# Kernel tuning notes

Hardware: AMD Instinct MI355X
Metric: run time of the kernel (lower is better)

The kernel has to match this reference:

```python
import jax, jax.numpy as jnp
import numpy as np

B, S, C, HD = 2, 1024, 1024, 64
H = C // HD  # 16 heads
E = 4
EPS = 1e-5


def _ln(x, g, b):
    m = jnp.mean(x, axis=-1, keepdims=True)
    v = jnp.mean(jnp.square(x - m), axis=-1, keepdims=True)
    return (x - m) / jnp.sqrt(v + EPS) * g + b


def setup_inputs() -> dict:
    key = jax.random.key(0)
    ks = jax.random.split(key, 16)
    s = 0.02
    return {
        "fwd_x": jax.random.normal(ks[0], (B, S + 1, C), jnp.float32),
        "bwd_x": jax.random.normal(ks[1], (B, S + 1, C), jnp.float32),
        "pos_embed": jax.random.normal(ks[2], (S, HD), jnp.float32) * 0.01,
        "ln1_g": jnp.ones((C,), jnp.float32),
        "ln1_b": jnp.zeros((C,), jnp.float32),
        "Wq": jax.random.normal(ks[3], (C, C), jnp.float32) * s,
        "bq": jnp.zeros((C,), jnp.float32),
        "Wk": jax.random.normal(ks[4], (C, C), jnp.float32) * s,
        "bk": jnp.zeros((C,), jnp.float32),
        "Wv": jax.random.normal(ks[5], (C, C), jnp.float32) * s,
        "bv": jnp.zeros((C,), jnp.float32),
        "Wo": jax.random.normal(ks[6], (C, C), jnp.float32) * s,
        "bo": jnp.zeros((C,), jnp.float32),
        "ln2_g": jnp.ones((C,), jnp.float32),
        "ln2_b": jnp.zeros((C,), jnp.float32),
        "mlp_g": jnp.ones((C,), jnp.float32),
        "mlp_b": jnp.zeros((C,), jnp.float32),
        "W1": jax.random.normal(ks[7], (C, E * C), jnp.float32) * s,
        "b1": jnp.zeros((E * C,), jnp.float32),
        "W2": jax.random.normal(ks[8], (E * C, C), jnp.float32) * s,
        "b2": jnp.zeros((C,), jnp.float32),
    }


def reference(fwd_x, bwd_x, pos_embed, ln1_g, ln1_b, Wq, bq, Wk, bk, Wv, bv,
              Wo, bo, ln2_g, ln2_b, mlp_g, mlp_b, W1, b1, W2, b2):
    f = fwd_x[:, :-1, :]   # [B, S, C]
    r = bwd_x[:, 1:, :]    # [B, S, C]
    comb = (f + r) * np.float32(1.0 / np.sqrt(2.0))

    all_embed = jnp.concatenate([f, r], axis=1)       # [B, 2S, C]
    cx = _ln(comb, ln1_g, ln1_b)
    ae = _ln(all_embed, ln1_g, ln1_b)

    q = (cx @ Wq + bq).reshape(B, S, H, HD)
    k = (ae @ Wk + bk).reshape(B, 2 * S, H, HD)
    v = (ae @ Wv + bv).reshape(B, 2 * S, H, HD)

    pos2 = jnp.concatenate([pos_embed, pos_embed], axis=0)  # [2S, HD]
    k = k + pos2[None, :, None, :]
    q = (q + pos_embed[None, :, None, :]) * np.float32(1.0 / np.sqrt(HD))

    logits = jnp.einsum('bqhd,bkhd->bhqk', q, k)      # [B, H, S, 2S]

    qi = jnp.arange(S)[:, None]
    ki = jnp.arange(S)[None, :]
    l2r = ki <= qi   # causal (keys up to and incl. q) on first half
    r2l = ki >= qi   # anti-causal on second half
    mask = jnp.concatenate([l2r, r2l], axis=-1)        # [S, 2S]

    neg = jnp.finfo(logits.dtype).min
    attn = jax.nn.softmax(jnp.where(mask[None, None], logits, neg), axis=-1)

    o = jnp.einsum('bhqk,bkhd->bqhd', attn, v).reshape(B, S, C)
    o = o @ Wo + bo

    x = comb + o
    h = _ln(_ln(x, ln2_g, ln2_b), mlp_g, mlp_b)
    m = jax.nn.gelu(h @ W1 + b1, approximate=False) @ W2 + b2
    return x + m
```

## Files before the change

### kernel.cpp

```cpp
#include <hip/hip_runtime.h>
#include <hip/hip_bf16.h>
#include <cstdint>

#define DI __device__ __forceinline__

typedef unsigned short u16;
typedef __bf16 bf16x8 __attribute__((ext_vector_type(8)));
typedef float f32x4 __attribute__((ext_vector_type(4)));

constexpr int Bc  = 2;
constexpr int Sc  = 1024;
constexpr int Cc  = 1024;
constexpr int Hc  = 16;
constexpr int HDc = 64;
constexpr int S2c = 2048;
constexpr int ECc = 4096;
constexpr int BSc  = Bc * Sc;
constexpr int BS2c = Bc * S2c;

constexpr int EPI_KV = 0, EPI_Q = 1, EPI_O = 3, EPI_GELU = 4, EPI_FINAL = 5, EPI_PART = 6;

DI u16 f2b(float f) {
  __hip_bfloat16 h = __float2bfloat16(f);
  u16 u;
  __builtin_memcpy(&u, &h, 2);
  return u;
}

DI u16 f2b_fast(float f) {
  uint32_t u;
  __builtin_memcpy(&u, &f, 4);
  return (u16)((u + 0x8000u) >> 16);
}

DI void glds16(const void* g, void* l) {
  auto* lp = reinterpret_cast<__attribute__((address_space(3))) uint32_t*>(
      reinterpret_cast<uintptr_t>(l));
  __builtin_amdgcn_global_load_lds(
      reinterpret_cast<const __attribute__((address_space(1))) uint32_t*>(
          reinterpret_cast<uintptr_t>(g)),
      lp, 16, 0, 0);
}

DI f32x4 mfma16(bf16x8 a, bf16x8 b, f32x4 c) {
  return __builtin_amdgcn_mfma_f32_16x16x32_bf16(a, b, c, 0, 0, 0);
}

#define PIPE_WAIT(N)                                            \
  do {                                                          \
    asm volatile("s_waitcnt vmcnt(" #N ")" ::: "memory");       \
    __builtin_amdgcn_sched_barrier(0);                          \
  } while (0)
#define PIPE_BAR()                                              \
  do {                                                          \
    __builtin_amdgcn_s_barrier();                               \
    __builtin_amdgcn_sched_barrier(0);                          \
  } while (0)

__global__ __launch_bounds__(256) void transpose4_kernel(const float* __restrict__ Wq,
                                                         const float* __restrict__ Wk,
                                                         const float* __restrict__ Wv,
                                                         const float* __restrict__ Wo,
                                                         u16* __restrict__ WqT,
                                                         u16* __restrict__ WkvT,
                                                         u16* __restrict__ WoT) {
  __shared__ float tile[32][33];
  const int z = blockIdx.z;
  const float* W = (z == 0) ? Wq : (z == 1) ? Wk : (z == 2) ? Wv : Wo;
  u16* WT = (z == 0) ? WqT : (z == 1) ? WkvT : (z == 2) ? (WkvT + (size_t)Cc * Cc) : WoT;
  const int bx = blockIdx.x, by = blockIdx.y;
  const int tx = threadIdx.x, ty = threadIdx.y;
  const int c = bx * 32 + tx;
#pragma unroll
  for (int i = ty; i < 32; i += 8) tile[i][tx] = W[(size_t)(by * 32 + i) * Cc + c];
  __syncthreads();
#pragma unroll
  for (int i = ty; i < 32; i += 8)
    WT[(size_t)(bx * 32 + i) * Cc + by * 32 + tx] = f2b(tile[tx][i]);
}

__global__ __launch_bounds__(256) void transpose_kernel(const float* __restrict__ W,
                                                        u16* __restrict__ WT, int R, int Cn) {
  __shared__ float tile[32][33];
  const int bx = blockIdx.x, by = blockIdx.y;
  const int tx = threadIdx.x, ty = threadIdx.y;
  const int c = bx * 32 + tx;
#pragma unroll
  for (int i = ty; i < 32; i += 8) tile[i][tx] = W[(size_t)(by * 32 + i) * Cn + c];
  __syncthreads();
#pragma unroll
  for (int i = ty; i < 32; i += 8)
    WT[(size_t)(bx * 32 + i) * R + by * 32 + tx] = f2b(tile[tx][i]);
}

__global__ __launch_bounds__(256) void prep_ln_kernel(
    const float* __restrict__ fwd, const float* __restrict__ bwd, const float* __restrict__ g,
    const float* __restrict__ be, float* __restrict__ comb, u16* __restrict__ cx,
    u16* __restrict__ ae) {
  __shared__ float red[2][4];
  const int row = blockIdx.x, tid = threadIdx.x;
  const int c = tid * 4;
  float4 x;
  u16* dst;
  if (row < BSc) {
    const int b = row >> 10, s = row & (Sc - 1);
    const float4 f = *(const float4*)(fwd + ((size_t)(b * (Sc + 1) + s)) * Cc + c);
    const float4 r = *(const float4*)(bwd + ((size_t)(b * (Sc + 1) + s + 1)) * Cc + c);
    const float k = 0.70710678118654752f;
    x.x = (f.x + r.x) * k; x.y = (f.y + r.y) * k;
    x.z = (f.z + r.z) * k; x.w = (f.w + r.w) * k;
    *(float4*)(comb + (size_t)row * Cc + c) = x;
    dst = cx + (size_t)row * Cc;
  } else {
    const int idx = row - BSc;
    const int b = idx >> 11, t = idx & (S2c - 1);
    const float* src = (t < Sc) ? (fwd + ((size_t)(b * (Sc + 1) + t)) * Cc)
                                : (bwd + ((size_t)(b * (Sc + 1) + (t - Sc) + 1)) * Cc);
    x = *(const float4*)(src + c);
    dst = ae + (size_t)idx * Cc;
  }
  float s1 = x.x + x.y + x.z + x.w;
  float s2 = x.x * x.x + x.y * x.y + x.z * x.z + x.w * x.w;
  for (int off = 32; off; off >>= 1) { s1 += __shfl_down(s1, off); s2 += __shfl_down(s2, off); }
  if ((tid & 63) == 0) { red[0][tid >> 6] = s1; red[1][tid >> 6] = s2; }
  __syncthreads();
  s1 = red[0][0] + red[0][1] + red[0][2] + red[0][3];
  s2 = red[1][0] + red[1][1] + red[1][2] + red[1][3];
  const float mean = s1 * (1.0f / Cc);
  const float rstd = rsqrtf(s2 * (1.0f / Cc) - mean * mean + 1e-5f);
  const float4 gv = *(const float4*)(g + c);
  const float4 bv = *(const float4*)(be + c);
  ushort4 o;
  o.x = f2b((x.x - mean) * rstd * gv.x + bv.x);
  o.y = f2b((x.y - mean) * rstd * gv.y + bv.y);
  o.z = f2b((x.z - mean) * rstd * gv.z + bv.z);
  o.w = f2b((x.w - mean) * rstd * gv.w + bv.w);
  *(ushort4*)(dst + c) = o;
}

__global__ __launch_bounds__(256) void ln2_kernel(const float* __restrict__ x,
                                                  const float* __restrict__ g2,
                                                  const float* __restrict__ b2,
                                                  const float* __restrict__ gm,
                                                  const float* __restrict__ bm,
                                                  u16* __restrict__ h) {
  __shared__ float red[2][4];
  const int row = blockIdx.x, tid = threadIdx.x;
  const int c = tid * 4;
  const float4 v = *(const float4*)(x + (size_t)row * Cc + c);
  float s1 = v.x + v.y + v.z + v.w;
  float s2 = v.x * v.x + v.y * v.y + v.z * v.z + v.w * v.w;
  for (int off = 32; off; off >>= 1) { s1 += __shfl_down(s1, off); s2 += __shfl_down(s2, off); }
  if ((tid & 63) == 0) { red[0][tid >> 6] = s1; red[1][tid >> 6] = s2; }
  __syncthreads();
  s1 = red[0][0] + red[0][1] + red[0][2] + red[0][3];
  s2 = red[1][0] + red[1][1] + red[1][2] + red[1][3];
  float mean = s1 * (1.0f / Cc);
  float rstd = rsqrtf(s2 * (1.0f / Cc) - mean * mean + 1e-5f);
  const float4 ga = *(const float4*)(g2 + c);
  const float4 ba = *(const float4*)(b2 + c);
  const float t0 = (v.x - mean) * rstd * ga.x + ba.x;
  const float t1 = (v.y - mean) * rstd * ga.y + ba.y;
  const float t2 = (v.z - mean) * rstd * ga.z + ba.z;
  const float t3 = (v.w - mean) * rstd * ga.w + ba.w;
  s1 = t0 + t1 + t2 + t3;
  s2 = t0 * t0 + t1 * t1 + t2 * t2 + t3 * t3;
  for (int off = 32; off; off >>= 1) { s1 += __shfl_down(s1, off); s2 += __shfl_down(s2, off); }
  __syncthreads();
  if ((tid & 63) == 0) { red[0][tid >> 6] = s1; red[1][tid >> 6] = s2; }
  __syncthreads();
  s1 = red[0][0] + red[0][1] + red[0][2] + red[0][3];
  s2 = red[1][0] + red[1][1] + red[1][2] + red[1][3];
  mean = s1 * (1.0f / Cc);
  rstd = rsqrtf(s2 * (1.0f / Cc) - mean * mean + 1e-5f);
  const float4 gb = *(const float4*)(gm + c);
  const float4 bb = *(const float4*)(bm + c);
  ushort4 o;
  o.x = f2b((t0 - mean) * rstd * gb.x + bb.x);
  o.y = f2b((t1 - mean) * rstd * gb.y + bb.y);
  o.z = f2b((t2 - mean) * rstd * gb.z + bb.z);
  o.w = f2b((t3 - mean) * rstd * gb.w + bb.w);
  *(ushort4*)(h + (size_t)row * Cc + c) = o;
}

template <int EPI, int SK>
__global__ __launch_bounds__(512) void gemm_kernel(
    const u16* __restrict__ A, const u16* __restrict__ BT, const float* __restrict__ bias,
    const float* __restrict__ bias2, const float* __restrict__ pos,
    u16* __restrict__ outb, u16* __restrict__ out2, float* __restrict__ pbuf,
    int M, int N, int K) {
  __shared__ u16 A0s[128 * 32], A1s[128 * 32], A2s[128 * 32], A3s[128 * 32];
  __shared__ u16 B0s[128 * 32], B1s[128 * 32], B2s[128 * 32], B3s[128 * 32];
  const int tid = threadIdx.x;
  const int w = tid >> 6, lane = tid & 63, quad = lane >> 4, r16 = lane & 15;
  const int bm = blockIdx.y * 128, bn = blockIdx.x * 128;
  const int wm = (w >> 2) * 64, wn = (w & 3) * 32;
  const int Ks = K / SK, kb0 = blockIdx.z * Ks;

  const int srow = tid >> 2, scol = (tid & 3) * 8;
  const u16* aP = A + (size_t)(bm + srow) * K + kb0 + scol;
  const u16* bP = BT + (size_t)(bn + srow) * K + kb0 + scol;
  const int stg = (w * 16) * 32;

  f32x4 acc[4][2] = {};

  auto STAGE = [&](u16* Ad, u16* Bd, int t) {
    const int ko = t * 32;
    glds16(aP + ko, Ad + stg);
    glds16(bP + ko, Bd + stg);
  };
  auto COMPUTE = [&](const u16* As, const u16* Bs) {
    bf16x8 af[4], bfr[2];
#pragma unroll
    for (int i = 0; i < 4; i++)
      af[i] = *reinterpret_cast<const bf16x8*>(&As[(wm + i * 16 + r16) * 32 + quad * 8]);
#pragma unroll
    for (int i = 0; i < 2; i++)
      bfr[i] = *reinterpret_cast<const bf16x8*>(&Bs[(wn + i * 16 + r16) * 32 + quad * 8]);
#pragma unroll
    for (int mi = 0; mi < 4; mi++)
#pragma unroll
      for (int ni = 0; ni < 2; ni++) acc[mi][ni] = mfma16(af[mi], bfr[ni], acc[mi][ni]);
  };

  const int NT = Ks / 32;
  STAGE(A0s, B0s, 0);
  STAGE(A1s, B1s, 1);
  for (int t = 0; t < NT; t += 4) {
    if (t + 2 < NT) { STAGE(A2s, B2s, t + 2); PIPE_WAIT(4); }
    else if (t + 1 < NT) PIPE_WAIT(2);
    else PIPE_WAIT(0);
    PIPE_BAR();
    COMPUTE(A0s, B0s);
    if (t + 3 < NT) { STAGE(A3s, B3s, t + 3); PIPE_WAIT(4); }
    else if (t + 2 < NT) PIPE_WAIT(2);
    else PIPE_WAIT(0);
    PIPE_BAR();
    COMPUTE(A1s, B1s);
    if (t + 4 < NT) { STAGE(A0s, B0s, t + 4); PIPE_WAIT(4); }
    else if (t + 3 < NT) PIPE_WAIT(2);
    else PIPE_WAIT(0);
    PIPE_BAR();
    COMPUTE(A2s, B2s);
    if (t + 5 < NT) { STAGE(A1s, B1s, t + 5); PIPE_WAIT(4); }
    else if (t + 4 < NT) PIPE_WAIT(2);
    else PIPE_WAIT(0);
    PIPE_BAR();
    COMPUTE(A3s, B3s);
  }

#pragma unroll
  for (int mi = 0; mi < 4; mi++) {
#pragma unroll
    for (int ni = 0; ni < 2; ni++) {
      const int col = bn + wn + ni * 16 + r16;
      const int row0 = bm + wm + mi * 16 + quad * 4;
      if constexpr (EPI == EPI_PART) {
        float* pb = pbuf + (size_t)blockIdx.z * M * N;
#pragma unroll
        for (int r = 0; r < 4; r++) pb[(size_t)(row0 + r) * N + col] = acc[mi][ni][r];
      } else if constexpr (EPI == EPI_KV) {
        if (col < Cc) {
#pragma unroll
          for (int r = 0; r < 4; r++) {
            const int row = row0 + r;
            const int key = row & (S2c - 1);
            const float y =
                acc[mi][ni][r] + bias[col] + pos[(key & (Sc - 1)) * HDc + (col & 63)];
            outb[(size_t)row * Cc + col] = f2b(y);
          }
        } else {
          const int c2 = col - Cc;
          const int h = c2 >> 6, d = c2 & 63;
          const int b = row0 >> 11, key0 = row0 & (S2c - 1);
          const float bb = bias2[c2];
          ushort4 pk;
          pk.x = f2b(acc[mi][ni][0] + bb);
          pk.y = f2b(acc[mi][ni][1] + bb);
          pk.z = f2b(acc[mi][ni][2] + bb);
          pk.w = f2b(acc[mi][ni][3] + bb);
          *(ushort4*)&out2[(((size_t)(b * Hc + h) * HDc + d) << 11) + key0] = pk;
        }
      } else {
#pragma unroll
        for (int r = 0; r < 4; r++) {
          const float y = acc[mi][ni][r] + bias[col];
          outb[(size_t)(row0 + r) * N + col] =
              f2b(0.5f * y * (1.0f + erff(y * 0.70710678118654752f)));
        }
      }
    }
  }
}

template <int EPI, int SK>
__global__ __launch_bounds__(256) void reduce_kernel(const float* __restrict__ pbuf,
                                                     const float* __restrict__ bias,
                                                     const float* __restrict__ pos,
                                                     const float* __restrict__ addsrc,
                                                     u16* __restrict__ outb,
                                                     float* __restrict__ outf, int M, int N) {
  const size_t flat = ((size_t)blockIdx.x * 256 + threadIdx.x) * 4;
  const int row = (int)(flat / N), col = (int)(flat % N);
  const size_t MN = (size_t)M * N;
  float4 s = *(const float4*)(pbuf + flat);
#pragma unroll
  for (int z = 1; z < SK; z++) {
    const float4 v = *(const float4*)(pbuf + z * MN + flat);
    s.x += v.x; s.y += v.y; s.z += v.z; s.w += v.w;
  }
  const float4 bv = *(const float4*)(bias + col);
  s.x += bv.x; s.y += bv.y; s.z += bv.z; s.w += bv.w;
  if constexpr (EPI == EPI_Q) {
    const int sq = row & (Sc - 1), d = col & 63;
    const float4 pv = *(const float4*)(pos + sq * HDc + d);
    constexpr float sc = 0.180336880111120426f;
    ushort4 o;
    o.x = f2b((s.x + pv.x) * sc);
    o.y = f2b((s.y + pv.y) * sc);
    o.z = f2b((s.z + pv.z) * sc);
    o.w = f2b((s.w + pv.w) * sc);
    *(ushort4*)(outb + flat) = o;
  } else {
    const float4 av = *(const float4*)(addsrc + flat);
    float4 o;
    o.x = s.x + av.x; o.y = s.y + av.y; o.z = s.z + av.z; o.w = s.w + av.w;
    *(float4*)(outf + flat) = o;
  }
}

__global__ __launch_bounds__(256) void attn_kernel(const u16* __restrict__ qb,
                                                   const u16* __restrict__ kb,
                                                   const u16* __restrict__ vT,
                                                   u16* __restrict__ ob) {
  const int bh = blockIdx.x;
  const int qt = blockIdx.y;
  const int b = bh >> 4, head = bh & 15;
  const int tid = threadIdx.x;
  const int w = tid >> 6, lane = tid & 63, quad = lane >> 4, r16 = lane & 15;

  __shared__ u16 K0s[4096], K1s[4096], K2s[4096], K3s[4096];
  __shared__ u16 V0s[4096], V1s[4096], V2s[4096], V3s[4096];
  __shared__ u16 Ps[4][16 * 68];
  u16* ps = Ps[w];

  const int qw = qt * 64 + w * 16;

  bf16x8 aq[2];
  {
    const u16* qp = qb + ((size_t)((b * Sc + qw + r16) * Hc + head)) * HDc + quad * 8;
    aq[0] = *(const bf16x8*)qp;
    aq[1] = *(const bf16x8*)(qp + 32);
  }

  const size_t krow = (size_t)Hc * HDc;
  const u16* kbase = kb + ((size_t)b * S2c * Hc + head) * HDc;
  const u16* vbase = vT + ((size_t)(b * Hc + head)) * HDc * S2c;

  const int srow = w * 16 + (lane >> 2);
  const int scol = (lane & 3) * 8;
  const int stg = w * 16 * 32;
  const u16* kS = kbase + (size_t)srow * krow + scol;
  const u16* vS = vbase + (size_t)srow * S2c + scol;

  f32x4 o_acc[4] = {};
  float lsum[4] = {};

  auto K0OF = [&](int p) -> int { return (p <= qt) ? p * 64 : Sc + (p - 1) * 64; };

  auto STAGE = [&](u16* Kd, u16* Vd, int p) {
    const int k0 = K0OF(p);
    glds16(kS + (size_t)k0 * krow, Kd + stg);
    glds16(kS + (size_t)k0 * krow + 32, Kd + 2048 + stg);
    glds16(vS + k0, Vd + stg);
    glds16(vS + k0 + 32, Vd + 2048 + stg);
  };

  auto COMPUTE = [&](const u16* Kc, const u16* Vc, int p) {
    const int k0 = K0OF(p);
    f32x4 sacc[4] = {};
#pragma unroll
    for (int ks = 0; ks < 2; ks++)
#pragma unroll
      for (int ni = 0; ni < 4; ni++) {
        const bf16x8 bk = *(const bf16x8*)&Kc[ks * 2048 + (ni * 16 + r16) * 32 + quad * 8];
        sacc[ni] = mfma16(aq[ks], bk, sacc[ni]);
      }
    const int mode = (p == qt) ? 1 : ((p == qt + 1) ? 2 : 0);
#pragma unroll
    for (int r = 0; r < 4; r++) {
      const int qrow = qw + quad * 4 + r;
#pragma unroll
      for (int ni = 0; ni < 4; ni++) {
        float s = sacc[ni][r];
        if (mode == 1) { const int key = k0 + ni * 16 + r16; if (key > qrow) s = -128.0f; }
        else if (mode == 2) { const int key = k0 - Sc + ni * 16 + r16; if (key < qrow) s = -128.0f; }
        const float pe = __builtin_amdgcn_exp2f(s);
        lsum[r] += pe;
        ps[(quad * 4 + r) * 68 + ni * 16 + r16] = f2b_fast(pe);
      }
    }
#pragma unroll
    for (int ks = 0; ks < 2; ks++) {
      const bf16x8 ap = *(const bf16x8*)(&ps[r16 * 68 + ks * 32 + quad * 8]);
#pragma unroll
      for (int ni = 0; ni < 4; ni++) {
        const bf16x8 bv_ = *(const bf16x8*)&Vc[ks * 2048 + (ni * 16 + r16) * 32 + quad * 8];
        o_acc[ni] = mfma16(ap, bv_, o_acc[ni]);
      }
    }
  };

  constexpr int NU = 17;
  STAGE(K0s, V0s, 0);
  STAGE(K1s, V1s, 1);
  for (int t = 0; t < NU; t += 4) {
    {
      if (t + 2 < NU) { STAGE(K2s, V2s, t + 2); PIPE_WAIT(8); }
      else if (t + 1 < NU) PIPE_WAIT(4);
      else PIPE_WAIT(0);
      PIPE_BAR();
      COMPUTE(K0s, V0s, t);
    }
    if (t + 1 < NU) {
      if (t + 3 < NU) { STAGE(K3s, V3s, t + 3); PIPE_WAIT(8); }
      else if (t + 2 < NU) PIPE_WAIT(4);
      else PIPE_WAIT(0);
      PIPE_BAR();
      COMPUTE(K1s, V1s, t + 1);
    }
    if (t + 2 < NU) {
      if (t + 4 < NU) { STAGE(K0s, V0s, t + 4); PIPE_WAIT(8); }
      else if (t + 3 < NU) PIPE_WAIT(4);
      else PIPE_WAIT(0);
      PIPE_BAR();
      COMPUTE(K2s, V2s, t + 2);
    }
    if (t + 3 < NU) {
      if (t + 5 < NU) { STAGE(K1s, V1s, t + 5); PIPE_WAIT(8); }
      else if (t + 4 < NU) PIPE_WAIT(4);
      else PIPE_WAIT(0);
      PIPE_BAR();
      COMPUTE(K3s, V3s, t + 3);
    }
  }

#pragma unroll
  for (int r = 0; r < 4; r++) {
    float l = lsum[r];
    l += __shfl_xor(l, 1);
    l += __shfl_xor(l, 2);
    l += __shfl_xor(l, 4);
    l += __shfl_xor(l, 8);
    lsum[r] = 1.0f / l;
  }
#pragma unroll
  for (int r = 0; r < 4; r++) {
    u16* od = ob + ((size_t)((b * Sc + qw + quad * 4 + r) * Hc + head)) * HDc;
#pragma unroll
    for (int ni = 0; ni < 4; ni++) od[ni * 16 + r16] = f2b(o_acc[ni][r] * lsum[r]);
  }
}

extern "C" void kernel_launch(void* const* d_in, const int* in_sizes, int n_in, void* d_out,
                              int out_size, void* d_ws, size_t ws_size, hipStream_t stream) {
  const float* fwd = (const float*)d_in[0];
  const float* bwd = (const float*)d_in[1];
  const float* pos = (const float*)d_in[2];
  const float* ln1g = (const float*)d_in[3];
  const float* ln1b = (const float*)d_in[4];
  const float* Wq = (const float*)d_in[5];
  const float* bq = (const float*)d_in[6];
  const float* Wk = (const float*)d_in[7];
  const float* bk = (const float*)d_in[8];
  const float* Wv = (const float*)d_in[9];
  const float* bv = (const float*)d_in[10];
  const float* Wo = (const float*)d_in[11];
  const float* bo = (const float*)d_in[12];
  const float* ln2g = (const float*)d_in[13];
  const float* ln2b = (const float*)d_in[14];
  const float* mlpg = (const float*)d_in[15];
  const float* mlpb = (const float*)d_in[16];
  const float* W1 = (const float*)d_in[17];
  const float* b1 = (const float*)d_in[18];
  const float* W2 = (const float*)d_in[19];
  const float* b2 = (const float*)d_in[20];

  char* p = (char*)d_ws;
  auto alloc = [&](size_t bytes) -> char* {
    char* r = p;
    p += (bytes + 255) & ~(size_t)255;
    return r;
  };
  float* comb = (float*)alloc((size_t)BSc * Cc * 4);
  float* xbuf = (float*)alloc((size_t)BSc * Cc * 4);
  u16* cx = (u16*)alloc((size_t)BSc * Cc * 2);
  u16* ae = (u16*)alloc((size_t)BS2c * Cc * 2);
  u16* qbuf = (u16*)alloc((size_t)BSc * Cc * 2);
  u16* kbuf = (u16*)alloc((size_t)BS2c * Cc * 2);
  u16* vTb = (u16*)alloc((size_t)BS2c * Cc * 2);
  u16* obuf = (u16*)alloc((size_t)BSc * Cc * 2);
  u16* hb = (u16*)alloc((size_t)BSc * Cc * 2);
  u16* midb = (u16*)alloc((size_t)BSc * ECc * 2);
  float* pbuf = (float*)alloc((size_t)4 * BSc * Cc * 4);
  u16* WqT = (u16*)alloc((size_t)Cc * Cc * 2);
  u16* WkvT = (u16*)alloc((size_t)2 * Cc * Cc * 2);
  u16* WoT = (u16*)alloc((size_t)Cc * Cc * 2);
  u16* W1T = (u16*)alloc((size_t)ECc * Cc * 2);
  u16* W2T = (u16*)alloc((size_t)Cc * ECc * 2);

  const dim3 tb(32, 8);
  transpose4_kernel<<<dim3(32, 32, 4), tb, 0, stream>>>(Wq, Wk, Wv, Wo, WqT, WkvT, WoT);
  transpose_kernel<<<dim3(128, 32), tb, 0, stream>>>(W1, W1T, Cc, ECc);
  transpose_kernel<<<dim3(32, 128), tb, 0, stream>>>(W2, W2T, ECc, Cc);

  prep_ln_kernel<<<BSc + BS2c, 256, 0, stream>>>(fwd, bwd, ln1g, ln1b, comb, cx, ae);

  gemm_kernel<EPI_PART, 4><<<dim3(Cc / 128, BSc / 128, 4), 512, 0, stream>>>(
      cx, WqT, nullptr, nullptr, nullptr, nullptr, nullptr, pbuf, BSc, Cc, Cc);
  reduce_kernel<EPI_Q, 4><<<(BSc * Cc / 4) / 256, 256, 0, stream>>>(
      pbuf, bq, pos, nullptr, qbuf, nullptr, BSc, Cc);

  gemm_kernel<EPI_KV, 1><<<dim3(2 * Cc / 128, BS2c / 128, 1), 512, 0, stream>>>(
      ae, WkvT, bk, bv, pos, kbuf, vTb, nullptr, BS2c, 2 * Cc, Cc);

  attn_kernel<<<dim3(Bc * Hc, Sc / 64), 256, 0, stream>>>(qbuf, kbuf, vTb, obuf);

  gemm_kernel<EPI_PART, 4><<<dim3(Cc / 128, BSc / 128, 4), 512, 0, stream>>>(
      obuf, WoT, nullptr, nullptr, nullptr, nullptr, nullptr, pbuf, BSc, Cc, Cc);
  reduce_kernel<EPI_O, 4><<<(BSc * Cc / 4) / 256, 256, 0, stream>>>(
      pbuf, bo, nullptr, comb, nullptr, xbuf, BSc, Cc);

  ln2_kernel<<<BSc, 256, 0, stream>>>(xbuf, ln2g, ln2b, mlpg, mlpb, hb);

  gemm_kernel<EPI_GELU, 1><<<dim3(ECc / 128, BSc / 128, 1), 512, 0, stream>>>(
      hb, W1T, b1, nullptr, nullptr, midb, nullptr, nullptr, BSc, ECc, Cc);

  gemm_kernel<EPI_PART, 4><<<dim3(Cc / 128, BSc / 128, 4), 512, 0, stream>>>(
      midb, W2T, nullptr, nullptr, nullptr, nullptr, nullptr, pbuf, BSc, Cc, ECc);
  reduce_kernel<EPI_FINAL, 4><<<(BSc * Cc / 4) / 256, 256, 0, stream>>>(
      pbuf, b2, nullptr, xbuf, nullptr, (float*)d_out, BSc, Cc);
}
```

Measured before the change: 322.0 us.

## Fuse O-projection split-K reduce into LN2 and use 1024-thread GEMM blocks

Merges the split-K reduction of the output projection (with bias and residual add) into the double-LayerNorm kernel, dropping one launch and one full read of the residual buffer. Separately, the GEMM moves from 512 to 1024 threads per 128x128 tile. Each wave now computes a 32x32 sub-tile instead of 64x32, and the A and B staging loads are split between two thread halves, so the pipeline wait counts are halved. The larger blocks raise wave count per tile but halve per-wave MFMA work and may cost occupancy or register headroom.

```diff
diff --git a/kernel.cpp b/kernel.cpp
--- a/kernel.cpp
+++ b/kernel.cpp
@@ -18,7 +18,7 @@
 constexpr int BSc  = Bc * Sc;
 constexpr int BS2c = Bc * S2c;
 
-constexpr int EPI_KV = 0, EPI_Q = 1, EPI_O = 3, EPI_GELU = 4, EPI_FINAL = 5, EPI_PART = 6;
+constexpr int EPI_KV = 0, EPI_Q = 1, EPI_GELU = 4, EPI_FINAL = 5, EPI_PART = 6;
 
 DI u16 f2b(float f) {
   __hip_bfloat16 h = __float2bfloat16(f);
@@ -138,18 +138,28 @@
   *(ushort4*)(dst + c) = o;
 }
 
-__global__ __launch_bounds__(256) void ln2_kernel(const float* __restrict__ x,
-                                                  const float* __restrict__ g2,
-                                                  const float* __restrict__ b2,
-                                                  const float* __restrict__ gm,
-                                                  const float* __restrict__ bm,
-                                                  u16* __restrict__ h) {
+__global__ __launch_bounds__(256) void reduceO_ln2_kernel(
+    const float* __restrict__ pbuf, const float* __restrict__ bo,
+    const float* __restrict__ comb, const float* __restrict__ g2,
+    const float* __restrict__ b2, const float* __restrict__ gm,
+    const float* __restrict__ bm, float* __restrict__ xbuf, u16* __restrict__ hb) {
   __shared__ float red[2][4];
   const int row = blockIdx.x, tid = threadIdx.x;
   const int c = tid * 4;
-  const float4 v = *(const float4*)(x + (size_t)row * Cc + c);
-  float s1 = v.x + v.y + v.z + v.w;
-  float s2 = v.x * v.x + v.y * v.y + v.z * v.z + v.w * v.w;
+  constexpr size_t MN = (size_t)BSc * Cc;
+  const size_t flat = (size_t)row * Cc + c;
+  float4 s = *(const float4*)(pbuf + flat);
+#pragma unroll
+  for (int z = 1; z < 4; z++) {
+    const float4 v = *(const float4*)(pbuf + z * MN + flat);
+    s.x += v.x; s.y += v.y; s.z += v.z; s.w += v.w;
+  }
+  const float4 bv = *(const float4*)(bo + c);
+  const float4 cv = *(const float4*)(comb + flat);
+  s.x += bv.x + cv.x; s.y += bv.y + cv.y; s.z += bv.z + cv.z; s.w += bv.w + cv.w;
+  *(float4*)(xbuf + flat) = s;
+  float s1 = s.x + s.y + s.z + s.w;
+  float s2 = s.x * s.x + s.y * s.y + s.z * s.z + s.w * s.w;
   for (int off = 32; off; off >>= 1) { s1 += __shfl_down(s1, off); s2 += __shfl_down(s2, off); }
   if ((tid & 63) == 0) { red[0][tid >> 6] = s1; red[1][tid >> 6] = s2; }
   __syncthreads();
@@ -159,10 +169,10 @@
   float rstd = rsqrtf(s2 * (1.0f / Cc) - mean * mean + 1e-5f);
   const float4 ga = *(const float4*)(g2 + c);
   const float4 ba = *(const float4*)(b2 + c);
-  const float t0 = (v.x - mean) * rstd * ga.x + ba.x;
-  const float t1 = (v.y - mean) * rstd * ga.y + ba.y;
-  const float t2 = (v.z - mean) * rstd * ga.z + ba.z;
-  const float t3 = (v.w - mean) * rstd * ga.w + ba.w;
+  const float t0 = (s.x - mean) * rstd * ga.x + ba.x;
+  const float t1 = (s.y - mean) * rstd * ga.y + ba.y;
+  const float t2 = (s.z - mean) * rstd * ga.z + ba.z;
+  const float t3 = (s.w - mean) * rstd * ga.w + ba.w;
   s1 = t0 + t1 + t2 + t3;
   s2 = t0 * t0 + t1 * t1 + t2 * t2 + t3 * t3;
   for (int off = 32; off; off >>= 1) { s1 += __shfl_down(s1, off); s2 += __shfl_down(s2, off); }
@@ -180,11 +190,11 @@
   o.y = f2b((t1 - mean) * rstd * gb.y + bb.y);
   o.z = f2b((t2 - mean) * rstd * gb.z + bb.z);
   o.w = f2b((t3 - mean) * rstd * gb.w + bb.w);
-  *(ushort4*)(h + (size_t)row * Cc + c) = o;
+  *(ushort4*)(hb + flat) = o;
 }
 
 template <int EPI, int SK>
-__global__ __launch_bounds__(512) void gemm_kernel(
+__global__ __launch_bounds__(1024) void gemm_kernel(
     const u16* __restrict__ A, const u16* __restrict__ BT, const float* __restrict__ bias,
     const float* __restrict__ bias2, const float* __restrict__ pos,
     u16* __restrict__ outb, u16* __restrict__ out2, float* __restrict__ pbuf,
@@ -194,31 +204,30 @@
   const int tid = threadIdx.x;
   const int w = tid >> 6, lane = tid & 63, quad = lane >> 4, r16 = lane & 15;
   const int bm = blockIdx.y * 128, bn = blockIdx.x * 128;
-  const int wm = (w >> 2) * 64, wn = (w & 3) * 32;
+  const int wm = ((w >> 2) & 3) * 32, wn = (w & 3) * 32;
   const int Ks = K / SK, kb0 = blockIdx.z * Ks;
 
-  const int srow = tid >> 2, scol = (tid & 3) * 8;
-  const u16* aP = A + (size_t)(bm + srow) * K + kb0 + scol;
-  const u16* bP = BT + (size_t)(bn + srow) * K + kb0 + scol;
-  const int stg = (w * 16) * 32;
-
-  f32x4 acc[4][2] = {};
+  const bool isB = (tid >= 512);
+  const int t2 = tid & 511;
+  const int srow = t2 >> 2, scol = (t2 & 3) * 8;
+  const u16* gP =
+      (isB ? BT + (size_t)(bn + srow) * K : A + (size_t)(bm + srow) * K) + kb0 + scol;
+  const int stg = ((w & 7) * 16) * 32;
+
+  f32x4 acc[2][2] = {};
 
   auto STAGE = [&](u16* Ad, u16* Bd, int t) {
-    const int ko = t * 32;
-    glds16(aP + ko, Ad + stg);
-    glds16(bP + ko, Bd + stg);
+    glds16(gP + t * 32, (isB ? Bd : Ad) + stg);
   };
   auto COMPUTE = [&](const u16* As, const u16* Bs) {
-    bf16x8 af[4], bfr[2];
-#pragma unroll
-    for (int i = 0; i < 4; i++)
+    bf16x8 af[2], bfr[2];
+#pragma unroll
+    for (int i = 0; i < 2; i++) {
       af[i] = *reinterpret_cast<const bf16x8*>(&As[(wm + i * 16 + r16) * 32 + quad * 8]);
-#pragma unroll
-    for (int i = 0; i < 2; i++)
       bfr[i] = *reinterpret_cast<const bf16x8*>(&Bs[(wn + i * 16 + r16) * 32 + quad * 8]);
-#pragma unroll
-    for (int mi = 0; mi < 4; mi++)
+    }
+#pragma unroll
+    for (int mi = 0; mi < 2; mi++)
 #pragma unroll
       for (int ni = 0; ni < 2; ni++) acc[mi][ni] = mfma16(af[mi], bfr[ni], acc[mi][ni]);
   };
@@ -227,30 +236,30 @@
   STAGE(A0s, B0s, 0);
   STAGE(A1s, B1s, 1);
   for (int t = 0; t < NT; t += 4) {
-    if (t + 2 < NT) { STAGE(A2s, B2s, t + 2); PIPE_WAIT(4); }
-    else if (t + 1 < NT) PIPE_WAIT(2);
+    if (t + 2 < NT) { STAGE(A2s, B2s, t + 2); PIPE_WAIT(2); }
+    else if (t + 1 < NT) PIPE_WAIT(1);
     else PIPE_WAIT(0);
     PIPE_BAR();
     COMPUTE(A0s, B0s);
-    if (t + 3 < NT) { STAGE(A3s, B3s, t + 3); PIPE_WAIT(4); }
-    else if (t + 2 < NT) PIPE_WAIT(2);
+    if (t + 3 < NT) { STAGE(A3s, B3s, t + 3); PIPE_WAIT(2); }
+    else if (t + 2 < NT) PIPE_WAIT(1);
     else PIPE_WAIT(0);
     PIPE_BAR();
     COMPUTE(A1s, B1s);
-    if (t + 4 < NT) { STAGE(A0s, B0s, t + 4); PIPE_WAIT(4); }
-    else if (t + 3 < NT) PIPE_WAIT(2);
+    if (t + 4 < NT) { STAGE(A0s, B0s, t + 4); PIPE_WAIT(2); }
+    else if (t + 3 < NT) PIPE_WAIT(1);
     else PIPE_WAIT(0);
     PIPE_BAR();
     COMPUTE(A2s, B2s);
-    if (t + 5 < NT) { STAGE(A1s, B1s, t + 5); PIPE_WAIT(4); }
-    else if (t + 4 < NT) PIPE_WAIT(2);
+    if (t + 5 < NT) { STAGE(A1s, B1s, t + 5); PIPE_WAIT(2); }
+    else if (t + 4 < NT) PIPE_WAIT(1);
     else PIPE_WAIT(0);
     PIPE_BAR();
     COMPUTE(A3s, B3s);
   }
 
 #pragma unroll
-  for (int mi = 0; mi < 4; mi++) {
+  for (int mi = 0; mi < 2; mi++) {
 #pragma unroll
     for (int ni = 0; ni < 2; ni++) {
       const int col = bn + wn + ni * 16 + r16;
@@ -516,27 +525,25 @@
 
   prep_ln_kernel<<<BSc + BS2c, 256, 0, stream>>>(fwd, bwd, ln1g, ln1b, comb, cx, ae);
 
-  gemm_kernel<EPI_PART, 4><<<dim3(Cc / 128, BSc / 128, 4), 512, 0, stream>>>(
+  gemm_kernel<EPI_PART, 4><<<dim3(Cc / 128, BSc / 128, 4), 1024, 0, stream>>>(
       cx, WqT, nullptr, nullptr, nullptr, nullptr, nullptr, pbuf, BSc, Cc, Cc);
   reduce_kernel<EPI_Q, 4><<<(BSc * Cc / 4) / 256, 256, 0, stream>>>(
       pbuf, bq, pos, nullptr, qbuf, nullptr, BSc, Cc);
 
-  gemm_kernel<EPI_KV, 1><<<dim3(2 * Cc / 128, BS2c / 128, 1), 512, 0, stream>>>(
+  gemm_kernel<EPI_KV, 1><<<dim3(2 * Cc / 128, BS2c / 128, 1), 1024, 0, stream>>>(
       ae, WkvT, bk, bv, pos, kbuf, vTb, nullptr, BS2c, 2 * Cc, Cc);
 
   attn_kernel<<<dim3(Bc * Hc, Sc / 64), 256, 0, stream>>>(qbuf, kbuf, vTb, obuf);
 
-  gemm_kernel<EPI_PART, 4><<<dim3(Cc / 128, BSc / 128, 4), 512, 0, stream>>>(
+  gemm_kernel<EPI_PART, 4><<<dim3(Cc / 128, BSc / 128, 4), 1024, 0, stream>>>(
       obuf, WoT, nullptr, nullptr, nullptr, nullptr, nullptr, pbuf, BSc, Cc, Cc);
-  reduce_kernel<EPI_O, 4><<<(BSc * Cc / 4) / 256, 256, 0, stream>>>(
-      pbuf, bo, nullptr, comb, nullptr, xbuf, BSc, Cc);
-
-  ln2_kernel<<<BSc, 256, 0, stream>>>(xbuf, ln2g, ln2b, mlpg, mlpb, hb);
-
-  gemm_kernel<EPI_GELU, 1><<<dim3(ECc / 128, BSc / 128, 1), 512, 0, stream>>>(
+  reduceO_ln2_kernel<<<BSc, 256, 0, stream>>>(pbuf, bo, comb, ln2g, ln2b, mlpg, mlpb,
+                                              xbuf, hb);
+
+  gemm_kernel<EPI_GELU, 1><<<dim3(ECc / 128, BSc / 128, 1), 1024, 0, stream>>>(
       hb, W1T, b1, nullptr, nullptr, midb, nullptr, nullptr, BSc, ECc, Cc);
 
-  gemm_kernel<EPI_PART, 4><<<dim3(Cc / 128, BSc / 128, 4), 512, 0, stream>>>(
+  gemm_kernel<EPI_PART, 4><<<dim3(Cc / 128, BSc / 128, 4), 1024, 0, stream>>>(
       midb, W2T, nullptr, nullptr, nullptr, nullptr, nullptr, pbuf, BSc, Cc, ECc);
   reduce_kernel<EPI_FINAL, 4><<<(BSc * Cc / 4) / 256, 256, 0, stream>>>(
       pbuf, b2, nullptr, xbuf, nullptr, (float*)d_out, BSc, Cc);
```

New measurement: 321.6 us. Within noise of the previous version (-0.1%).

## Replace split-K GEMM plus reduce with 64x64 intra-block split-K GEMM

Applied to the files above, without the earlier changes.

Removes the global split-K path, where four fp32 partial buffers were written and then summed by a separate reduce kernel, for the Q, O and W2 projections. It adds a 64x64-tile GEMM in which two groups of four waves each take half of K, with partials combined through LDS and bias/pos/residual applied in the epilogue. This drops the large fp32 partial-buffer traffic and extra launches, at the cost of smaller tiles with less reuse per block and per-element scalar stores.

```diff
diff --git a/kernel.cpp b/kernel.cpp
--- a/kernel.cpp
+++ b/kernel.cpp
@@ -18,7 +18,7 @@
 constexpr int BSc  = Bc * Sc;
 constexpr int BS2c = Bc * S2c;
 
-constexpr int EPI_KV = 0, EPI_Q = 1, EPI_O = 3, EPI_GELU = 4, EPI_FINAL = 5, EPI_PART = 6;
+constexpr int EPI_KV = 0, EPI_Q = 1, EPI_O = 3, EPI_GELU = 4, EPI_FINAL = 5;
 
 DI u16 f2b(float f) {
   __hip_bfloat16 h = __float2bfloat16(f);
@@ -54,6 +54,11 @@
 #define PIPE_BAR()                                              \
   do {                                                          \
     __builtin_amdgcn_s_barrier();                               \
+    __builtin_amdgcn_sched_barrier(0);                          \
+  } while (0)
+#define LGKM_FENCE()                                            \
+  do {                                                          \
+    asm volatile("s_waitcnt lgkmcnt(0)" ::: "memory");          \
     __builtin_amdgcn_sched_barrier(0);                          \
   } while (0)
 
@@ -183,23 +188,21 @@
   *(ushort4*)(h + (size_t)row * Cc + c) = o;
 }
 
-template <int EPI, int SK>
+template <int EPI>
 __global__ __launch_bounds__(512) void gemm_kernel(
     const u16* __restrict__ A, const u16* __restrict__ BT, const float* __restrict__ bias,
     const float* __restrict__ bias2, const float* __restrict__ pos,
-    u16* __restrict__ outb, u16* __restrict__ out2, float* __restrict__ pbuf,
-    int M, int N, int K) {
+    u16* __restrict__ outb, u16* __restrict__ out2, int M, int N, int K) {
   __shared__ u16 A0s[128 * 32], A1s[128 * 32], A2s[128 * 32], A3s[128 * 32];
   __shared__ u16 B0s[128 * 32], B1s[128 * 32], B2s[128 * 32], B3s[128 * 32];
   const int tid = threadIdx.x;
   const int w = tid >> 6, lane = tid & 63, quad = lane >> 4, r16 = lane & 15;
   const int bm = blockIdx.y * 128, bn = blockIdx.x * 128;
   const int wm = (w >> 2) * 64, wn = (w & 3) * 32;
-  const int Ks = K / SK, kb0 = blockIdx.z * Ks;
 
   const int srow = tid >> 2, scol = (tid & 3) * 8;
-  const u16* aP = A + (size_t)(bm + srow) * K + kb0 + scol;
-  const u16* bP = BT + (size_t)(bn + srow) * K + kb0 + scol;
+  const u16* aP = A + (size_t)(bm + srow) * K + scol;
+  const u16* bP = BT + (size_t)(bn + srow) * K + scol;
   const int stg = (w * 16) * 32;
 
   f32x4 acc[4][2] = {};
@@ -223,7 +226,7 @@
       for (int ni = 0; ni < 2; ni++) acc[mi][ni] = mfma16(af[mi], bfr[ni], acc[mi][ni]);
   };
 
-  const int NT = Ks / 32;
+  const int NT = K / 32;
   STAGE(A0s, B0s, 0);
   STAGE(A1s, B1s, 1);
   for (int t = 0; t < NT; t += 4) {
@@ -255,11 +258,7 @@
     for (int ni = 0; ni < 2; ni++) {
       const int col = bn + wn + ni * 16 + r16;
       const int row0 = bm + wm + mi * 16 + quad * 4;
-      if constexpr (EPI == EPI_PART) {
-        float* pb = pbuf + (size_t)blockIdx.z * M * N;
-#pragma unroll
-        for (int r = 0; r < 4; r++) pb[(size_t)(row0 + r) * N + col] = acc[mi][ni][r];
-      } else if constexpr (EPI == EPI_KV) {
+      if constexpr (EPI == EPI_KV) {
         if (col < Cc) {
 #pragma unroll
           for (int r = 0; r < 4; r++) {
@@ -293,39 +292,106 @@
   }
 }
 
-template <int EPI, int SK>
-__global__ __launch_bounds__(256) void reduce_kernel(const float* __restrict__ pbuf,
-                                                     const float* __restrict__ bias,
-                                                     const float* __restrict__ pos,
-                                                     const float* __restrict__ addsrc,
-                                                     u16* __restrict__ outb,
-                                                     float* __restrict__ outf, int M, int N) {
-  const size_t flat = ((size_t)blockIdx.x * 256 + threadIdx.x) * 4;
-  const int row = (int)(flat / N), col = (int)(flat % N);
-  const size_t MN = (size_t)M * N;
-  float4 s = *(const float4*)(pbuf + flat);
-#pragma unroll
-  for (int z = 1; z < SK; z++) {
-    const float4 v = *(const float4*)(pbuf + z * MN + flat);
-    s.x += v.x; s.y += v.y; s.z += v.z; s.w += v.w;
-  }
-  const float4 bv = *(const float4*)(bias + col);
-  s.x += bv.x; s.y += bv.y; s.z += bv.z; s.w += bv.w;
-  if constexpr (EPI == EPI_Q) {
-    const int sq = row & (Sc - 1), d = col & 63;
-    const float4 pv = *(const float4*)(pos + sq * HDc + d);
-    constexpr float sc = 0.180336880111120426f;
-    ushort4 o;
-    o.x = f2b((s.x + pv.x) * sc);
-    o.y = f2b((s.y + pv.y) * sc);
-    o.z = f2b((s.z + pv.z) * sc);
-    o.w = f2b((s.w + pv.w) * sc);
-    *(ushort4*)(outb + flat) = o;
-  } else {
-    const float4 av = *(const float4*)(addsrc + flat);
-    float4 o;
-    o.x = s.x + av.x; o.y = s.y + av.y; o.z = s.z + av.z; o.w = s.w + av.w;
-    *(float4*)(outf + flat) = o;
+template <int EPI>
+__global__ __launch_bounds__(512) void gemm64_kernel(
+    const u16* __restrict__ A, const u16* __restrict__ BT, const float* __restrict__ bias,
+    const float* __restrict__ pos, const float* __restrict__ addsrc,
+    u16* __restrict__ outb, float* __restrict__ outf, int M, int N, int K) {
+  __shared__ u16 A0s[128 * 32], A1s[128 * 32], A2s[128 * 32], A3s[128 * 32];
+  __shared__ u16 B0s[128 * 32], B1s[128 * 32], B2s[128 * 32], B3s[128 * 32];
+  const int tid = threadIdx.x;
+  const int w = tid >> 6, lane = tid & 63, quad = lane >> 4, r16 = lane & 15;
+  const int kh = w >> 2, qd = w & 3;
+  const int wm = (qd >> 1) * 32, wn = (qd & 1) * 32;
+  const int bm = blockIdx.y * 64, bn = blockIdx.x * 64;
+  const int K2 = K >> 1;
+
+  const int sr = (tid >> 2) & 63, sh = tid >> 8, scb = (tid & 3) * 8;
+  const u16* aP = A + (size_t)(bm + sr) * K + sh * K2 + scb;
+  const u16* bP = BT + (size_t)(bn + sr) * K + sh * K2 + scb;
+  const int stg = w * 512;
+
+  f32x4 acc[2][2] = {};
+
+  auto STAGE = [&](u16* Ad, u16* Bd, int t) {
+    glds16(aP + t * 32, Ad + stg);
+    glds16(bP + t * 32, Bd + stg);
+  };
+  auto COMPUTE = [&](const u16* As, const u16* Bs) {
+    bf16x8 af[2], bfr[2];
+#pragma unroll
+    for (int i = 0; i < 2; i++) {
+      af[i] = *reinterpret_cast<const bf16x8*>(
+          &As[(kh * 64 + wm + i * 16 + r16) * 32 + quad * 8]);
+      bfr[i] = *reinterpret_cast<const bf16x8*>(
+          &Bs[(kh * 64 + wn + i * 16 + r16) * 32 + quad * 8]);
+    }
+#pragma unroll
+    for (int mi = 0; mi < 2; mi++)
+#pragma unroll
+      for (int ni = 0; ni < 2; ni++) acc[mi][ni] = mfma16(af[mi], bfr[ni], acc[mi][ni]);
+  };
+
+  const int NT = K2 / 32;
+  STAGE(A0s, B0s, 0);
+  STAGE(A1s, B1s, 1);
+  for (int t = 0; t < NT; t += 4) {
+    if (t + 2 < NT) { STAGE(A2s, B2s, t + 2); PIPE_WAIT(4); }
+    else if (t + 1 < NT) PIPE_WAIT(2);
+    else PIPE_WAIT(0);
+    PIPE_BAR();
+    COMPUTE(A0s, B0s);
+    if (t + 3 < NT) { STAGE(A3s, B3s, t + 3); PIPE_WAIT(4); }
+    else if (t + 2 < NT) PIPE_WAIT(2);
+    else PIPE_WAIT(0);
+    PIPE_BAR();
+    COMPUTE(A1s, B1s);
+    if (t + 4 < NT) { STAGE(A0s, B0s, t + 4); PIPE_WAIT(4); }
+    else if (t + 3 < NT) PIPE_WAIT(2);
+    else PIPE_WAIT(0);
+    PIPE_BAR();
+    COMPUTE(A2s, B2s);
+    if (t + 5 < NT) { STAGE(A1s, B1s, t + 5); PIPE_WAIT(4); }
+    else if (t + 4 < NT) PIPE_WAIT(2);
+    else PIPE_WAIT(0);
+    PIPE_BAR();
+    COMPUTE(A3s, B3s);
+  }
+
+  PIPE_BAR();
+  float* rb = (qd < 2 ? (float*)A0s : (float*)A1s) + (qd & 1) * 1024;
+  if (kh == 1) {
+#pragma unroll
+    for (int mi = 0; mi < 2; mi++)
+#pragma unroll
+      for (int ni = 0; ni < 2; ni++)
+#pragma unroll
+        for (int r = 0; r < 4; r++)
+          rb[(mi * 16 + quad * 4 + r) * 32 + ni * 16 + r16] = acc[mi][ni][r];
+  }
+  LGKM_FENCE();
+  PIPE_BAR();
+  if (kh == 0) {
+#pragma unroll
+    for (int mi = 0; mi < 2; mi++)
+#pragma unroll
+      for (int ni = 0; ni < 2; ni++) {
+        const int col = bn + wn + ni * 16 + r16;
+        const float bcol = bias[col];
+#pragma unroll
+        for (int r = 0; r < 4; r++) {
+          const int row = bm + wm + mi * 16 + quad * 4 + r;
+          const float y =
+              acc[mi][ni][r] + rb[(mi * 16 + quad * 4 + r) * 32 + ni * 16 + r16] + bcol;
+          const size_t flat = (size_t)row * N + col;
+          if constexpr (EPI == EPI_Q) {
+            constexpr float scq = 0.180336880111120426f;
+            outb[flat] = f2b((y + pos[(row & (Sc - 1)) * HDc + (col & 63)]) * scq);
+          } else {
+            outf[flat] = y + addsrc[flat];
+          }
+        }
+      }
   }
 }
 
@@ -502,7 +568,6 @@
   u16* obuf = (u16*)alloc((size_t)BSc * Cc * 2);
   u16* hb = (u16*)alloc((size_t)BSc * Cc * 2);
   u16* midb = (u16*)alloc((size_t)BSc * ECc * 2);
-  float* pbuf = (float*)alloc((size_t)4 * BSc * Cc * 4);
   u16* WqT = (u16*)alloc((size_t)Cc * Cc * 2);
   u16* WkvT = (u16*)alloc((size_t)2 * Cc * Cc * 2);
   u16* WoT = (u16*)alloc((size_t)Cc * Cc * 2);
@@ -516,28 +581,22 @@
 
   prep_ln_kernel<<<BSc + BS2c, 256, 0, stream>>>(fwd, bwd, ln1g, ln1b, comb, cx, ae);
 
-  gemm_kernel<EPI_PART, 4><<<dim3(Cc / 128, BSc / 128, 4), 512, 0, stream>>>(
-      cx, WqT, nullptr, nullptr, nullptr, nullptr, nullptr, pbuf, BSc, Cc, Cc);
-  reduce_kernel<EPI_Q, 4><<<(BSc * Cc / 4) / 256, 256, 0, stream>>>(
-      pbuf, bq, pos, nullptr, qbuf, nullptr, BSc, Cc);
-
-  gemm_kernel<EPI_KV, 1><<<dim3(2 * Cc / 128, BS2c / 128, 1), 512, 0, stream>>>(
-      ae, WkvT, bk, bv, pos, kbuf, vTb, nullptr, BS2c, 2 * Cc, Cc);
+  gemm64_kernel<EPI_Q><<<dim3(Cc / 64, BSc / 64), 512, 0, stream>>>(
+      cx, WqT, bq, pos, nullptr, qbuf, nullptr, BSc, Cc, Cc);
+
+  gemm_kernel<EPI_KV><<<dim3(2 * Cc / 128, BS2c / 128), 512, 0, stream>>>(
+      ae, WkvT, bk, bv, pos, kbuf, vTb, BS2c, 2 * Cc, Cc);
 
   attn_kernel<<<dim3(Bc * Hc, Sc / 64), 256, 0, stream>>>(qbuf, kbuf, vTb, obuf);
 
-  gemm_kernel<EPI_PART, 4><<<dim3(Cc / 128, BSc / 128, 4), 512, 0, stream>>>(
-      obuf, WoT, nullptr, nullptr, nullptr, nullptr, nullptr, pbuf, BSc, Cc, Cc);
-  reduce_kernel<EPI_O, 4><<<(BSc * Cc / 4) / 256, 256, 0, stream>>>(
-      pbuf, bo, nullptr, comb, nullptr, xbuf, BSc, Cc);
+  gemm64_kernel<EPI_O><<<dim3(Cc / 64, BSc / 64), 512, 0, stream>>>(
+      obuf, WoT, bo, nullptr, comb, nullptr, xbuf, BSc, Cc, Cc);
 
   ln2_kernel<<<BSc, 256, 0, stream>>>(xbuf, ln2g, ln2b, mlpg, mlpb, hb);
 
-  gemm_kernel<EPI_GELU, 1><<<dim3(ECc / 128, BSc / 128, 1), 512, 0, stream>>>(
-      hb, W1T, b1, nullptr, nullptr, midb, nullptr, nullptr, BSc, ECc, Cc);
-
-  gemm_kernel<EPI_PART, 4><<<dim3(Cc / 128, BSc / 128, 4), 512, 0, stream>>>(
-      midb, W2T, nullptr, nullptr, nullptr, nullptr, nullptr, pbuf, BSc, Cc, ECc);
-  reduce_kernel<EPI_FINAL, 4><<<(BSc * Cc / 4) / 256, 256, 0, stream>>>(
-      pbuf, b2, nullptr, xbuf, nullptr, (float*)d_out, BSc, Cc);
-}
+  gemm_kernel<EPI_GELU><<<dim3(ECc / 128, BSc / 128), 512, 0, stream>>>(
+      hb, W1T, b1, nullptr, nullptr, midb, nullptr, BSc, ECc, Cc);
+
+  gemm64_kernel<EPI_FINAL><<<dim3(Cc / 64, BSc / 64), 512, 0, stream>>>(
+      midb, W2T, b2, nullptr, xbuf, nullptr, (float*)d_out, BSc, Cc, ECc);
+}
```

Result: faster. 307.6 us (-4.5%).
